# Kernel tuning notes

Hardware: AMD Instinct MI355X
Metric: run time of the kernel (lower is better)

## Reference

```python
import jax, jax.numpy as jnp
import numpy as np

BETA = 1.0
ALPHA = 0.5


def setup_inputs() -> dict:
    key = jax.random.key(0)
    k1, k2, k3 = jax.random.split(key, 3)
    B, N1, N2 = 512, 256, 32768
    v = jax.random.normal(k1, (B, N1), dtype=jnp.float32)
    mask = jax.random.uniform(k2, (B, N1), dtype=jnp.float32)
    Mem = jax.random.normal(k3, (N2, N1), dtype=jnp.float32)  # kernel [N2, N1] (trailing 1 squeezed)
    return {"v": v, "mask": mask, "Mem": Mem}


def reference(v, mask, Mem):
    # Squared L2 distance d2[i, b] = ||Mem[i] - v[b]||^2, computed without the
    # [N2, N1, B] diff tensor via the expansion ||m||^2 - 2 m.v + ||v||^2.
    m2 = jnp.sum(Mem * Mem, axis=1)            # [N2]
    v2 = jnp.sum(v * v, axis=1)                # [B]
    cross = jnp.einsum('nd,bd->nb', Mem, v)    # [N2, B]
    d2 = m2[:, None] - 2.0 * cross + v2[None, :]
    # Gaussian-kernel weights over the N2 stored patterns (softmax == exp/sum).
    w = jax.nn.softmax(-0.5 * BETA * d2, axis=0)  # [N2, B]
    # update[b] = sum_i w[i,b] * (Mem[i] - v[b]) = (w^T Mem)[b] - v[b]
    update = jnp.einsum('nb,nd->bd', w, Mem) - v   # [B, N1]
    return v + ALPHA * update * mask
```

## Files before the change

### kernel.cpp

```cpp
#include <hip/hip_runtime.h>
#include <hip/hip_bf16.h>
#include <stdint.h>

typedef float  f32x4  __attribute__((ext_vector_type(4)));
typedef float  f32x16 __attribute__((ext_vector_type(16)));
typedef _Float16 half8 __attribute__((ext_vector_type(8)));
typedef unsigned int uint32;

#define N1 256
#define N2T 32768
#define BQ 512
#define KT 32
#define TILE_B 16384


union H4 { _Float16 h[4]; unsigned short s[4]; uint2 u2; };

__global__ __launch_bounds__(256) void mhn_prep_k(
    const float* __restrict__ Mem, _Float16* __restrict__ rowF,
    _Float16* __restrict__ memF, float* __restrict__ m2g)
{
  const int t   = blockIdx.x;
  const int tid = threadIdx.x;
  const int a    = tid >> 4;
  const int dblk = tid & 15;
  const int r0i  = 32*t + 2*a;

  const float* p0 = Mem + (size_t)r0i*N1 + dblk*16;
  const float* p1 = p0 + N1;
  float4 x0[4], x1[4];
  #pragma unroll
  for (int i=0;i<4;i++){ x0[i] = *(const float4*)(p0+4*i); x1[i] = *(const float4*)(p1+4*i); }

  float s0=0.f, s1=0.f;
  H4 h0[4], h1[4];
  #pragma unroll
  for (int i=0;i<4;i++){
    s0 += x0[i].x*x0[i].x + x0[i].y*x0[i].y + x0[i].z*x0[i].z + x0[i].w*x0[i].w;
    s1 += x1[i].x*x1[i].x + x1[i].y*x1[i].y + x1[i].z*x1[i].z + x1[i].w*x1[i].w;
    h0[i].h[0]=(_Float16)x0[i].x; h0[i].h[1]=(_Float16)x0[i].y; h0[i].h[2]=(_Float16)x0[i].z; h0[i].h[3]=(_Float16)x0[i].w;
    h1[i].h[0]=(_Float16)x1[i].x; h1[i].h[1]=(_Float16)x1[i].y; h1[i].h[2]=(_Float16)x1[i].z; h1[i].h[3]=(_Float16)x1[i].w;
  }

  {
    char* bF = (char*)rowF + (size_t)t*TILE_B + dblk*1024;
    #pragma unroll
    for (int hi=0; hi<2; hi++){
      uint4 wa, wb;
      wa.x = h0[2*hi].u2.x;   wa.y = h0[2*hi].u2.y;
      wa.z = h0[2*hi+1].u2.x; wa.w = h0[2*hi+1].u2.y;
      wb.x = h1[2*hi].u2.x;   wb.y = h1[2*hi].u2.y;
      wb.z = h1[2*hi+1].u2.x; wb.w = h1[2*hi+1].u2.y;
      *(uint4*)(bF + (2*a  )*16 + hi*512) = wa;
      *(uint4*)(bF + (2*a+1)*16 + hi*512) = wb;
    }
  }

  {
    char* bM = (char*)memF + (size_t)t*TILE_B
             + (size_t)(2*(dblk>>1) + (a>>3))*1024
             + (size_t)((dblk&1)*16 + 32*((a>>2)&1))*16
             + (size_t)(a&3)*4;
    #pragma unroll
    for (int i=0;i<4;i++){
      #pragma unroll
      for (int j=0;j<4;j++){
        *(uint32*)(bM + (4*i+j)*16) = (uint32)h0[i].s[j] | ((uint32)h1[i].s[j] << 16);
      }
    }
  }

  s0 += __shfl_xor(s0,1); s0 += __shfl_xor(s0,2); s0 += __shfl_xor(s0,4); s0 += __shfl_xor(s0,8);
  s1 += __shfl_xor(s1,1); s1 += __shfl_xor(s1,2); s1 += __shfl_xor(s1,4); s1 += __shfl_xor(s1,8);
  if (dblk == 0){ m2g[r0i] = -0.5f*s0; m2g[r0i+1] = -0.5f*s1; }
}

__global__ __launch_bounds__(256, 2) void mhn_flash_k(
    const _Float16* __restrict__ rowF, const _Float16* __restrict__ memF,
    const float* __restrict__ m2g, const float* __restrict__ v,
    __hip_bfloat16* __restrict__ Opart, float* __restrict__ mpart,
    float* __restrict__ lpart, int CK, int nt)
{
  const int tid = threadIdx.x;
  const int w   = tid >> 6;
  const int l   = tid & 63;
  const int row = l & 31;
  const int hi  = l >> 5;

  const int nwg = gridDim.x;
  const int bid = blockIdx.x;
  const int s_  = (bid & 7) * (nwg >> 3) + (bid >> 3);
  const int c   = s_ >> 2;
  const int qb  = s_ & 3;
  const int tpc = CK >> 5;

  const char* gR = (const char*)rowF + (size_t)(c*tpc)*TILE_B + (uint32)l*16;
  const char* gT = (const char*)memF + (size_t)(c*tpc)*TILE_B + (uint32)l*16;

  half8 v8[16];
  const int q0 = qb*128 + w*32;
  {
    const float* vp = v + (size_t)(q0 + row)*N1 + 8*hi;
    #pragma unroll
    for (int s=0;s<16;s++){
      const float4 a = *(const float4*)(vp + 16*s);
      const float4 b = *(const float4*)(vp + 16*s + 4);
      half8 hv;
      hv[0]=(_Float16)a.x; hv[1]=(_Float16)a.y; hv[2]=(_Float16)a.z; hv[3]=(_Float16)a.w;
      hv[4]=(_Float16)b.x; hv[5]=(_Float16)b.y; hv[6]=(_Float16)b.z; hv[7]=(_Float16)b.w;
      v8[s]=hv;
    }
  }

  float mrun = -INFINITY, lrun = 0.f;
  f32x16 oacc[8];
  #pragma unroll
  for (int b=0;b<8;b++) oacc[b] = (f32x16)(0.f);

  const float* m2p = m2g + c*CK + 4*hi;

  for (int tt=0; tt<nt; ++tt){
    f32x4 m2v[4];
    #pragma unroll
    for (int b=0;b<4;b++) m2v[b] = *(const f32x4*)(m2p + 8*b);

    f32x16 S = (f32x16)(0.f);
    #pragma unroll
    for (int s=0;s<16;s++){
      const half8 a = *(const half8*)(gR + s*1024);
      S = __builtin_amdgcn_mfma_f32_32x32x16_f16(a, v8[s], S, 0,0,0);
    }
    gR += TILE_B;

    float p[16];
    #pragma unroll
    for (int r=0;r<16;r++) p[r] = S[r] + m2v[r>>2][r&3];

    float tm = p[0];
    #pragma unroll
    for (int r=1;r<16;r++) tm = fmaxf(tm, p[r]);
    tm = fmaxf(tm, __shfl_xor(tm, 32));
    if (__any(tm > mrun + 8.0f)){
      const float nm = fmaxf(mrun, tm);
      const float sc = __expf(mrun - nm);
      lrun *= sc; mrun = nm;
      #pragma unroll
      for (int b=0;b<8;b++) oacc[b] *= sc;
    }
    #pragma unroll
    for (int r=0;r<16;r++) p[r] = __expf(p[r] - mrun);

    uint32 D[8];
    #pragma unroll
    for (int i=0;i<8;i++){
      union { __fp16 h2 __attribute__((ext_vector_type(2))); uint32 u; } cv;
      cv.h2 = __builtin_amdgcn_cvt_pkrtz(p[2*i], p[2*i+1]);
      D[i] = cv.u;
    }
    uint32 wq[8];
    {
      const uint32 tD0 = (uint32)__shfl_xor((int)D[0], 32);
      const uint32 tD1 = (uint32)__shfl_xor((int)D[1], 32);
      const uint32 tD2 = (uint32)__shfl_xor((int)D[2], 32);
      const uint32 tD3 = (uint32)__shfl_xor((int)D[3], 32);
      const uint32 tD4 = (uint32)__shfl_xor((int)D[4], 32);
      const uint32 tD5 = (uint32)__shfl_xor((int)D[5], 32);
      const uint32 tD6 = (uint32)__shfl_xor((int)D[6], 32);
      const uint32 tD7 = (uint32)__shfl_xor((int)D[7], 32);
      const bool lo = (hi == 0);
      wq[0] = lo ? D[0] : tD2;  wq[1] = lo ? D[1] : tD3;
      wq[2] = lo ? tD0 : D[2];  wq[3] = lo ? tD1 : D[3];
      wq[4] = lo ? D[4] : tD6;  wq[5] = lo ? D[5] : tD7;
      wq[6] = lo ? tD4 : D[6];  wq[7] = lo ? tD5 : D[7];
    }
    union { uint32 u[4]; half8 h; } pb1, pb2;
    pb1.u[0]=wq[0]; pb1.u[1]=wq[1]; pb1.u[2]=wq[2]; pb1.u[3]=wq[3];
    pb2.u[0]=wq[4]; pb2.u[1]=wq[5]; pb2.u[2]=wq[6]; pb2.u[3]=wq[7];

    half8 A1 = *(const half8*)(gT);
    half8 A2 = *(const half8*)(gT + 1024);
    #pragma unroll
    for (int b=0;b<8;b++){
      half8 nA1, nA2;
      if (b < 7){
        nA1 = *(const half8*)(gT + (2*b+2)*1024);
        nA2 = *(const half8*)(gT + (2*b+3)*1024);
      }
      oacc[b] = __builtin_amdgcn_mfma_f32_32x32x16_f16(A1, pb1.h, oacc[b], 0,0,0);
      oacc[b] = __builtin_amdgcn_mfma_f32_32x32x16_f16(A2, pb2.h, oacc[b], 0,0,0);
      if (b < 7){ A1 = nA1; A2 = nA2; }
    }
    gT += TILE_B;

    float ps = 0.f;
    #pragma unroll
    for (int r=0;r<16;r++) ps += p[r];
    ps += __shfl_xor(ps, 32); lrun += ps;

    m2p += KT;
  }

  {
    __hip_bfloat16* Op = Opart + (size_t)c*N1*BQ + (q0 + row);
    #pragma unroll
    for (int b=0;b<8;b++){
      #pragma unroll
      for (int r=0;r<16;r++){
        const int d = 32*b + (r&3) + 8*(r>>2) + 4*hi;
        Op[(size_t)d*BQ] = __float2bfloat16(oacc[b][r]);
      }
    }
    if (hi == 0){
      mpart[(size_t)c*BQ + q0 + row] = mrun;
      lpart[(size_t)c*BQ + q0 + row] = lrun;
    }
  }
}

__global__ __launch_bounds__(256) void mhn_wprep_k(
    const float* __restrict__ mpart, const float* __restrict__ lpart,
    float* __restrict__ W, float* __restrict__ invL, int nchunk)
{
  __shared__ float sred[4];
  const int q = blockIdx.x;
  const int c = threadIdx.x;
  const int l = c & 63, wv = c >> 6;

  const float m = (c < nchunk) ? mpart[(size_t)c*BQ + q] : -INFINITY;
  const float lv = (c < nchunk) ? lpart[(size_t)c*BQ + q] : 0.f;

  float r = m;
  r = fmaxf(r, __shfl_xor(r,1));  r = fmaxf(r, __shfl_xor(r,2));
  r = fmaxf(r, __shfl_xor(r,4));  r = fmaxf(r, __shfl_xor(r,8));
  r = fmaxf(r, __shfl_xor(r,16)); r = fmaxf(r, __shfl_xor(r,32));
  if (l == 0) sred[wv] = r;
  __syncthreads();
  const float M = fmaxf(fmaxf(sred[0], sred[1]), fmaxf(sred[2], sred[3]));
  __syncthreads();

  const float e = __expf(m - M);
  float s = lv * e;
  s += __shfl_xor(s,1);  s += __shfl_xor(s,2);
  s += __shfl_xor(s,4);  s += __shfl_xor(s,8);
  s += __shfl_xor(s,16); s += __shfl_xor(s,32);
  if (l == 0) sred[wv] = s;
  __syncthreads();

  if (c < nchunk) W[(size_t)c*BQ + q] = e;
  if (c == 0) invL[q] = 1.0f / ((sred[0] + sred[1]) + (sred[2] + sred[3]));
}

__global__ __launch_bounds__(256) void mhn_wsum_k(
    const float* __restrict__ v, const float* __restrict__ mask,
    const __hip_bfloat16* __restrict__ Opart, const float* __restrict__ W,
    const float* __restrict__ invL, float* __restrict__ out, int nchunk)
{
  const int g  = blockIdx.x*256 + threadIdx.x;
  const int q2 = (g & 255) * 2;
  const int d  = g >> 8;

  const __hip_bfloat16* op = Opart + (size_t)d*BQ + q2;
  const float* wp = W + q2;
  float acc0 = 0.f, acc1 = 0.f;
  #pragma unroll 8
  for (int c2=0; c2<nchunk; c2++){
    const uint32 o2 = *(const uint32*)(op + (size_t)c2*N1*BQ);
    const float2 w2 = *(const float2*)(wp + (size_t)c2*BQ);
    acc0 += __bfloat162float(__hip_bfloat16_raw{(unsigned short)(o2 & 0xffffu)}) * w2.x;
    acc1 += __bfloat162float(__hip_bfloat16_raw{(unsigned short)(o2 >> 16)})     * w2.y;
  }
  const float2 iL = *(const float2*)(invL + q2);
  const size_t oi0 = (size_t)q2*N1 + d;
  const float vv0 = v[oi0], mk0 = mask[oi0];
  const float vv1 = v[oi0 + N1], mk1 = mask[oi0 + N1];
  out[oi0]      = vv0 + 0.5f*(acc0*iL.x - vv0)*mk0;
  out[oi0 + N1] = vv1 + 0.5f*(acc1*iL.y - vv1)*mk1;
}

extern "C" void kernel_launch(void* const* d_in, const int* in_sizes, int n_in,
                              void* d_out, int out_size, void* d_ws, size_t ws_size,
                              hipStream_t stream)
{
  (void)in_sizes; (void)n_in; (void)out_size;
  const float* v    = (const float*)d_in[0];
  const float* mask = (const float*)d_in[1];
  const float* Mem  = (const float*)d_in[2];
  float* out = (float*)d_out;

  const size_t fixedB   = (size_t)N2T*N1*2*2 + (size_t)N2T*4 + (size_t)BQ*4;
  const size_t perChunk = (size_t)BQ*N1*2 + (size_t)BQ*12;
  int nchunk = 128;
  while (nchunk > 4 && fixedB + (size_t)nchunk*perChunk > ws_size) nchunk >>= 1;

  char* wsb = (char*)d_ws;
  _Float16* rowF = (_Float16*)wsb;
  _Float16* memF = (_Float16*)(wsb + (size_t)N2T*N1*2);
  float*    m2g  = (float*)(wsb + (size_t)N2T*N1*4);
  float*    invL = (float*)(wsb + (size_t)N2T*N1*4 + (size_t)N2T*4);
  char* pb = wsb + fixedB;
  __hip_bfloat16* Opart = (__hip_bfloat16*)pb;
  float* mpart = (float*)(pb + (size_t)nchunk*BQ*N1*2);
  float* lpart = mpart + (size_t)nchunk*BQ;
  float* W     = lpart + (size_t)nchunk*BQ;

  const int CK = N2T / nchunk;
  const int nt = CK / KT;

  mhn_prep_k<<<dim3(N2T/KT), dim3(256), 0, stream>>>(Mem, rowF, memF, m2g);
  mhn_flash_k<<<dim3(4*nchunk), dim3(256), 0, stream>>>(rowF, memF, m2g, v, Opart, mpart, lpart, CK, nt);
  mhn_wprep_k<<<dim3(BQ), dim3(256), 0, stream>>>(mpart, lpart, W, invL, nchunk);
  mhn_wsum_k<<<dim3((N1*BQ)/512), dim3(256), 0, stream>>>(v, mask, Opart, W, invL, out, nchunk);
}
```

Baseline: 77.84 us.

## Split fused flash kernel into separate QK-softmax and PV kernels via fp16 P buffer

```diff
diff --git a/kernel.cpp b/kernel.cpp
--- a/kernel.cpp
+++ b/kernel.cpp
@@ -5,6 +5,7 @@
 typedef float  f32x4  __attribute__((ext_vector_type(4)));
 typedef float  f32x16 __attribute__((ext_vector_type(16)));
 typedef _Float16 half8 __attribute__((ext_vector_type(8)));
+typedef _Float16 half2v __attribute__((ext_vector_type(2)));
 typedef unsigned int uint32;
 
 #define N1 256
@@ -12,6 +13,7 @@
 #define BQ 512
 #define KT 32
 #define TILE_B 16384
+#define NTILE (N2T/KT)
 
 
 union H4 { _Float16 h[4]; unsigned short s[4]; uint2 u2; };
@@ -75,11 +77,10 @@
   if (dblk == 0){ m2g[r0i] = -0.5f*s0; m2g[r0i+1] = -0.5f*s1; }
 }
 
-__global__ __launch_bounds__(256, 2) void mhn_flash_k(
-    const _Float16* __restrict__ rowF, const _Float16* __restrict__ memF,
-    const float* __restrict__ m2g, const float* __restrict__ v,
-    __hip_bfloat16* __restrict__ Opart, float* __restrict__ mpart,
-    float* __restrict__ lpart, int CK, int nt)
+__global__ __launch_bounds__(256) void mhn_qk_k(
+    const _Float16* __restrict__ rowF, const float* __restrict__ m2g,
+    const float* __restrict__ v, _Float16* __restrict__ pF,
+    float* __restrict__ mt, float* __restrict__ lt)
 {
   const int tid = threadIdx.x;
   const int w   = tid >> 6;
@@ -87,18 +88,12 @@
   const int row = l & 31;
   const int hi  = l >> 5;
 
-  const int nwg = gridDim.x;
   const int bid = blockIdx.x;
-  const int s_  = (bid & 7) * (nwg >> 3) + (bid >> 3);
-  const int c   = s_ >> 2;
-  const int qb  = s_ & 3;
-  const int tpc = CK >> 5;
-
-  const char* gR = (const char*)rowF + (size_t)(c*tpc)*TILE_B + (uint32)l*16;
-  const char* gT = (const char*)memF + (size_t)(c*tpc)*TILE_B + (uint32)l*16;
+  const int qg  = (bid & 3)*4 + w;
+  const int t0  = (bid >> 2) * 2;
+  const int q0  = qg*32;
 
   half8 v8[16];
-  const int q0 = qb*128 + w*32;
   {
     const float* vp = v + (size_t)(q0 + row)*N1 + 8*hi;
     #pragma unroll
@@ -112,25 +107,21 @@
     }
   }
 
-  float mrun = -INFINITY, lrun = 0.f;
-  f32x16 oacc[8];
   #pragma unroll
-  for (int b=0;b<8;b++) oacc[b] = (f32x16)(0.f);
-
-  const float* m2p = m2g + c*CK + 4*hi;
-
-  for (int tt=0; tt<nt; ++tt){
+  for (int tt=0; tt<2; ++tt){
+    const int t = t0 + tt;
+    const float* m2p = m2g + t*KT + 4*hi;
     f32x4 m2v[4];
     #pragma unroll
     for (int b=0;b<4;b++) m2v[b] = *(const f32x4*)(m2p + 8*b);
 
+    const char* gR = (const char*)rowF + (size_t)t*TILE_B + (uint32)l*16;
     f32x16 S = (f32x16)(0.f);
     #pragma unroll
     for (int s=0;s<16;s++){
       const half8 a = *(const half8*)(gR + s*1024);
       S = __builtin_amdgcn_mfma_f32_32x32x16_f16(a, v8[s], S, 0,0,0);
     }
-    gR += TILE_B;
 
     float p[16];
     #pragma unroll
@@ -140,15 +131,12 @@
     #pragma unroll
     for (int r=1;r<16;r++) tm = fmaxf(tm, p[r]);
     tm = fmaxf(tm, __shfl_xor(tm, 32));
-    if (__any(tm > mrun + 8.0f)){
-      const float nm = fmaxf(mrun, tm);
-      const float sc = __expf(mrun - nm);
-      lrun *= sc; mrun = nm;
-      #pragma unroll
-      for (int b=0;b<8;b++) oacc[b] *= sc;
-    }
-    #pragma unroll
-    for (int r=0;r<16;r++) p[r] = __expf(p[r] - mrun);
+    #pragma unroll
+    for (int r=0;r<16;r++) p[r] = __expf(p[r] - tm);
+    float ps = 0.f;
+    #pragma unroll
+    for (int r=0;r<16;r++) ps += p[r];
+    ps += __shfl_xor(ps, 32);
 
     uint32 D[8];
     #pragma unroll
@@ -157,7 +145,7 @@
       cv.h2 = __builtin_amdgcn_cvt_pkrtz(p[2*i], p[2*i+1]);
       D[i] = cv.u;
     }
-    uint32 wq[8];
+    uint4 f1, f2;
     {
       const uint32 tD0 = (uint32)__shfl_xor((int)D[0], 32);
       const uint32 tD1 = (uint32)__shfl_xor((int)D[1], 32);
@@ -168,15 +156,71 @@
       const uint32 tD6 = (uint32)__shfl_xor((int)D[6], 32);
       const uint32 tD7 = (uint32)__shfl_xor((int)D[7], 32);
       const bool lo = (hi == 0);
-      wq[0] = lo ? D[0] : tD2;  wq[1] = lo ? D[1] : tD3;
-      wq[2] = lo ? tD0 : D[2];  wq[3] = lo ? tD1 : D[3];
-      wq[4] = lo ? D[4] : tD6;  wq[5] = lo ? D[5] : tD7;
-      wq[6] = lo ? tD4 : D[6];  wq[7] = lo ? tD5 : D[7];
-    }
-    union { uint32 u[4]; half8 h; } pb1, pb2;
-    pb1.u[0]=wq[0]; pb1.u[1]=wq[1]; pb1.u[2]=wq[2]; pb1.u[3]=wq[3];
-    pb2.u[0]=wq[4]; pb2.u[1]=wq[5]; pb2.u[2]=wq[6]; pb2.u[3]=wq[7];
-
+      f1.x = lo ? D[0] : tD2;  f1.y = lo ? D[1] : tD3;
+      f1.z = lo ? tD0 : D[2];  f1.w = lo ? tD1 : D[3];
+      f2.x = lo ? D[4] : tD6;  f2.y = lo ? D[5] : tD7;
+      f2.z = lo ? tD4 : D[6];  f2.w = lo ? tD5 : D[7];
+    }
+    char* pw = (char*)pF + ((size_t)(t*16 + qg))*2048 + (uint32)l*16;
+    *(uint4*)pw          = f1;
+    *(uint4*)(pw + 1024) = f2;
+
+    if (hi == 0){
+      mt[(size_t)t*BQ + q0 + row] = tm;
+      lt[(size_t)t*BQ + q0 + row] = ps;
+    }
+  }
+}
+
+__global__ __launch_bounds__(256) void mhn_pv_k(
+    const _Float16* __restrict__ memF, const _Float16* __restrict__ pF,
+    const float* __restrict__ mt, const float* __restrict__ lt,
+    __hip_bfloat16* __restrict__ Opart, float* __restrict__ mpart,
+    float* __restrict__ lpart, int nt)
+{
+  const int tid = threadIdx.x;
+  const int w   = tid >> 6;
+  const int l   = tid & 63;
+  const int row = l & 31;
+  const int hi  = l >> 5;
+
+  const int nwg = gridDim.x;
+  const int bid = blockIdx.x;
+  const int s_  = (bid & 7) * (nwg >> 3) + (bid >> 3);
+  const int c   = s_ >> 2;
+  const int qb  = s_ & 3;
+  const int qg  = qb*4 + w;
+  const int q0  = qg*32;
+
+  float Mrun = -INFINITY, Lrun = 0.f;
+  f32x16 oacc[8];
+  #pragma unroll
+  for (int b=0;b<8;b++) oacc[b] = (f32x16)(0.f);
+
+  const int tbase = c*nt;
+  for (int tti=0; tti<nt; ++tti){
+    const int t = tbase + tti;
+    const float mtv = mt[(size_t)t*BQ + q0 + row];
+    if (__any(mtv > Mrun + 8.0f)){
+      const float nm = fmaxf(Mrun, mtv);
+      const float sc = __expf(Mrun - nm);
+      Lrun *= sc; Mrun = nm;
+      #pragma unroll
+      for (int b=0;b<8;b++) oacc[b] *= sc;
+    }
+    const float g32 = __expf(mtv - Mrun);
+    Lrun += lt[(size_t)t*BQ + q0 + row] * g32;
+
+    const char* pw = (const char*)pF + ((size_t)(t*16 + qg))*2048 + (uint32)l*16;
+    union PU { uint4 q; half2v h2[4]; half8 h; } pb1, pb2;
+    pb1.q = *(const uint4*)pw;
+    pb2.q = *(const uint4*)(pw + 1024);
+    const _Float16 gh = (_Float16)g32;
+    half2v gv; gv[0] = gh; gv[1] = gh;
+    #pragma unroll
+    for (int i=0;i<4;i++){ pb1.h2[i] *= gv; pb2.h2[i] *= gv; }
+
+    const char* gT = (const char*)memF + (size_t)t*TILE_B + (uint32)l*16;
     half8 A1 = *(const half8*)(gT);
     half8 A2 = *(const half8*)(gT + 1024);
     #pragma unroll
@@ -190,14 +234,6 @@
       oacc[b] = __builtin_amdgcn_mfma_f32_32x32x16_f16(A2, pb2.h, oacc[b], 0,0,0);
       if (b < 7){ A1 = nA1; A2 = nA2; }
     }
-    gT += TILE_B;
-
-    float ps = 0.f;
-    #pragma unroll
-    for (int r=0;r<16;r++) ps += p[r];
-    ps += __shfl_xor(ps, 32); lrun += ps;
-
-    m2p += KT;
   }
 
   {
@@ -211,8 +247,8 @@
       }
     }
     if (hi == 0){
-      mpart[(size_t)c*BQ + q0 + row] = mrun;
-      lpart[(size_t)c*BQ + q0 + row] = lrun;
+      mpart[(size_t)c*BQ + q0 + row] = Mrun;
+      lpart[(size_t)c*BQ + q0 + row] = Lrun;
     }
   }
 }
@@ -287,27 +323,35 @@
   const float* Mem  = (const float*)d_in[2];
   float* out = (float*)d_out;
 
-  const size_t fixedB   = (size_t)N2T*N1*2*2 + (size_t)N2T*4 + (size_t)BQ*4;
+  const size_t rowFB = (size_t)N2T*N1*2;
+  const size_t memFB = (size_t)N2T*N1*2;
+  const size_t m2B   = (size_t)N2T*4;
+  const size_t pFB   = (size_t)N2T*BQ*2;
+  const size_t mtB   = (size_t)NTILE*BQ*4;
+  const size_t fixedB = rowFB + memFB + m2B + pFB + 2*mtB + (size_t)BQ*4;
   const size_t perChunk = (size_t)BQ*N1*2 + (size_t)BQ*12;
-  int nchunk = 128;
+  int nchunk = 64;
   while (nchunk > 4 && fixedB + (size_t)nchunk*perChunk > ws_size) nchunk >>= 1;
 
   char* wsb = (char*)d_ws;
   _Float16* rowF = (_Float16*)wsb;
-  _Float16* memF = (_Float16*)(wsb + (size_t)N2T*N1*2);
-  float*    m2g  = (float*)(wsb + (size_t)N2T*N1*4);
-  float*    invL = (float*)(wsb + (size_t)N2T*N1*4 + (size_t)N2T*4);
+  _Float16* memF = (_Float16*)(wsb + rowFB);
+  float*    m2g  = (float*)(wsb + rowFB + memFB);
+  _Float16* pF   = (_Float16*)(wsb + rowFB + memFB + m2B);
+  float*    mt   = (float*)(wsb + rowFB + memFB + m2B + pFB);
+  float*    lt   = (float*)(wsb + rowFB + memFB + m2B + pFB + mtB);
+  float*    invL = (float*)(wsb + rowFB + memFB + m2B + pFB + 2*mtB);
   char* pb = wsb + fixedB;
   __hip_bfloat16* Opart = (__hip_bfloat16*)pb;
   float* mpart = (float*)(pb + (size_t)nchunk*BQ*N1*2);
   float* lpart = mpart + (size_t)nchunk*BQ;
   float* W     = lpart + (size_t)nchunk*BQ;
 
-  const int CK = N2T / nchunk;
-  const int nt = CK / KT;
-
-  mhn_prep_k<<<dim3(N2T/KT), dim3(256), 0, stream>>>(Mem, rowF, memF, m2g);
-  mhn_flash_k<<<dim3(4*nchunk), dim3(256), 0, stream>>>(rowF, memF, m2g, v, Opart, mpart, lpart, CK, nt);
+  const int nt = (N2T / nchunk) / KT;
+
+  mhn_prep_k<<<dim3(NTILE), dim3(256), 0, stream>>>(Mem, rowF, memF, m2g);
+  mhn_qk_k<<<dim3(NTILE*2), dim3(256), 0, stream>>>(rowF, m2g, v, pF, mt, lt);
+  mhn_pv_k<<<dim3(4*nchunk), dim3(256), 0, stream>>>(memF, pF, mt, lt, Opart, mpart, lpart, nt);
   mhn_wprep_k<<<dim3(BQ), dim3(256), 0, stream>>>(mpart, lpart, W, invL, nchunk);
   mhn_wsum_k<<<dim3((N1*BQ)/512), dim3(256), 0, stream>>>(v, mask, Opart, W, invL, out, nchunk);
 }
```

After: 130.7 us. 67.9% more time.
